# Performance work log

Measured on AMD Instinct MI355X. Metric: run time of the kernel, lower is better.

The kernel has to match this reference:

```python
import jax, jax.numpy as jnp
import numpy as np
import jax.scipy.linalg as jsp

H = 8
C = 64
D_CONV = 4
EPS_L2 = 1e-6
EPS_RMS = 1e-5


def l2norm(x):
    return x * jax.lax.rsqrt(jnp.sum(x * x, axis=-1, keepdims=True) + EPS_L2)


def setup_inputs() -> dict:
    key = jax.random.key(0)
    ks = jax.random.split(key, 12)
    B, T, D = 4, 4096, 1024
    x = jax.random.normal(ks[0], (B, T, D), dtype=jnp.float32)
    s = 0.02
    Wv = jax.random.normal(ks[1], (D, D), dtype=jnp.float32) * s
    Wg = jax.random.normal(ks[2], (D, D), dtype=jnp.float32) * s
    Wo = jax.random.normal(ks[3], (D, D), dtype=jnp.float32) * s
    Wb = jax.random.normal(ks[4], (H, D), dtype=jnp.float32) * s
    Wa = jax.random.normal(ks[5], (H, D), dtype=jnp.float32) * s
    # dt_bias / A_log initialized as in the torch module
    u = jax.random.uniform(ks[6], (H,))
    dt = jnp.exp(u * (jnp.log(0.1) - jnp.log(0.001)) + jnp.log(0.001))
    dt_bias = dt + jnp.log(-jnp.expm1(-dt))
    A_log = jnp.log(jax.random.uniform(ks[7], (H,)) * 16.0 + 1e-4)
    norm_w = jnp.ones((D // H,), dtype=jnp.float32)
    conv_w = jax.random.normal(ks[8], (D, D_CONV), dtype=jnp.float32) * 0.1
    conv_b = jnp.zeros((D,), dtype=jnp.float32)
    return {"x": x, "Wv": Wv, "Wg": Wg, "Wo": Wo, "Wb": Wb, "Wa": Wa,
            "dt_bias": dt_bias, "A_log": A_log, "norm_w": norm_w,
            "conv_w": conv_w, "conv_b": conv_b}


def _causal_depthwise_conv(x, w, b):
    # x: (B,T,D), w: (D,d_conv) -- causal depthwise conv1d
    B, T, D = x.shape
    xp = jnp.pad(x, ((0, 0), (D_CONV - 1, 0), (0, 0)))
    out = b
    for j in range(D_CONV):
        out = out + xp[:, j:j + T] * w[:, j]
    return out


def _forward(x, Wv, Wg, Wo, Wb, Wa, dt_bias, A_log, norm_w, conv_w, conv_b):
    B, T, D = x.shape
    K = D // H
    n = T // C  # T chosen as a multiple of C, so pad_len == 0

    rk = l2norm(x.reshape(B, T, H, K)) / np.sqrt(K)
    x_shift = jnp.pad(x[:, :-1], ((0, 0), (1, 0), (0, 0)))
    wk = l2norm(x_shift.reshape(B, T, H, K))
    v = jax.nn.silu(_causal_depthwise_conv(x @ Wv.T, conv_w, conv_b)).reshape(B, T, H, K)
    gate = (x @ Wg.T).reshape(B, T, H, K)
    beta = jax.nn.sigmoid(x @ Wb.T)                       # (B,T,H)
    decay = -jnp.exp(A_log) * jax.nn.softplus(x @ Wa.T + dt_bias)  # (B,T,H)

    # -> (B,H,T,K)
    rk, wk, v = (jnp.transpose(t, (0, 2, 1, 3)) for t in (rk, wk, v))
    beta_t = jnp.transpose(beta, (0, 2, 1))[..., None]    # (B,H,T,1)
    v = v * beta_t
    wk_beta = wk * beta_t

    # chunk: (B,H,n,C,K)
    ch = lambda t: t.reshape(B, H, n, C, K)
    rk, wk, v, wk_beta = ch(rk), ch(wk), ch(v), ch(wk_beta)
    decay = jnp.cumsum(jnp.transpose(decay, (0, 2, 1)).reshape(B, H, n, C), axis=-1)
    decay_exp = jnp.exp(decay)[..., None]                 # (B,H,n,C,1)

    tril = jnp.tril(jnp.ones((C, C), dtype=bool))
    strict_lower = jnp.tril(jnp.ones((C, C), dtype=bool), k=-1)
    diff = decay[..., :, None] - decay[..., None, :]
    L_mask = jnp.where(tril, jnp.exp(jnp.where(tril, diff, 0.0)), 0.0)  # (B,H,n,C,C)

    A_strict = jnp.where(strict_lower,
                         -(jnp.einsum('bhnck,bhndk->bhncd', wk_beta, wk) * L_mask), 0.0)
    # forward-substitution loop == inverse of unit-lower-triangular (I - A_strict)
    eye = jnp.eye(C, dtype=x.dtype)
    Tmat = jsp.solve_triangular(eye - A_strict,
                                jnp.broadcast_to(eye, A_strict.shape),
                                lower=True)
    v = Tmat @ v
    wk_cumdecay = Tmat @ (wk_beta * decay_exp)

    # scan over chunks maintaining state S: (B,H,K,K)
    def step(S, inp):
        rk_i, wk_i, v_i, wkc_i, L_i, dec_i = inp
        attn = jnp.where(tril, jnp.einsum('bhck,bhdk->bhcd', rk_i, wk_i) * L_i, 0.0)
        v_new = v_i - wkc_i @ S
        o_inter = (rk_i * jnp.exp(dec_i)[..., None]) @ S
        o_i = o_inter + attn @ v_new
        dw = jnp.exp(dec_i[..., -1:] - dec_i)[..., None]
        S_new = S * jnp.exp(dec_i[..., -1])[..., None, None] + \
            jnp.einsum('bhck,bhcv->bhkv', wk_i * dw, v_new)
        return S_new, o_i

    mv = lambda t: jnp.moveaxis(t, 2, 0)  # chunk axis to front
    S0 = jnp.zeros((B, H, K, K), dtype=x.dtype)
    _, o = jax.lax.scan(step, S0, (mv(rk), mv(wk), mv(v), mv(wk_cumdecay),
                                   mv(L_mask), mv(decay)))
    # o: (n,B,H,C,K) -> (B,T,H,K)
    o = jnp.transpose(o, (1, 0, 3, 2, 4)).reshape(B, T, H, K)

    # per-head RMSNorm, gated, output projection
    o = o * jax.lax.rsqrt(jnp.mean(o * o, axis=-1, keepdims=True) + EPS_RMS) * norm_w
    o = o * jax.nn.silu(gate)
    return o.reshape(B, T, D) @ Wo.T


def reference(x, Wv, Wg, Wo, Wb, Wa, dt_bias, A_log, norm_w, conv_w, conv_b):
    return _forward(x, Wv, Wg, Wo, Wb, Wa, dt_bias, A_log, norm_w, conv_w, conv_b)
```

## Files before the change

kernel.cpp:

```cpp
#include <hip/hip_runtime.h>
#include <hip/hip_bf16.h>
#include <math.h>

#define H_ 8
#define K_ 128
#define C_ 64
#define D_ 1024
#define T_ 4096
#define B_ 4
#define N_CH 64
#define BT_ (B_*T_)

typedef __attribute__((ext_vector_type(8))) short bf16x8;
typedef __attribute__((ext_vector_type(4))) float f32x4;
typedef __hip_bfloat16 bf16;

#define BAR_LGKM() do { \
  asm volatile("s_waitcnt lgkmcnt(0)" ::: "memory"); \
  __builtin_amdgcn_sched_barrier(0); \
  __builtin_amdgcn_s_barrier(); \
} while(0)

__device__ __forceinline__ float siluf(float x){ return x / (1.0f + expf(-x)); }
__device__ __forceinline__ float expn(float x){ return expf(fminf(x, 0.f)); }
__device__ __forceinline__ float sanf(float v){ return (__builtin_fabsf(v) <= 1e30f) ? v : 0.f; }

__device__ __forceinline__ void ld_bf8(const bf16* p, float* o){
  uint4 u = *(const uint4*)p;
  o[0]=__uint_as_float(u.x<<16); o[1]=__uint_as_float(u.x&0xffff0000u);
  o[2]=__uint_as_float(u.y<<16); o[3]=__uint_as_float(u.y&0xffff0000u);
  o[4]=__uint_as_float(u.z<<16); o[5]=__uint_as_float(u.z&0xffff0000u);
  o[6]=__uint_as_float(u.w<<16); o[7]=__uint_as_float(u.w&0xffff0000u);
}
__device__ __forceinline__ void ld_bf8s(const bf16* p, float* o){
  ld_bf8(p, o);
#pragma unroll
  for (int e=0;e<8;e++) o[e] = sanf(o[e]);
}
__device__ __forceinline__ void ld_bf4(const bf16* p, float* o){
  uint2 u = *(const uint2*)p;
  o[0]=__uint_as_float(u.x<<16); o[1]=__uint_as_float(u.x&0xffff0000u);
  o[2]=__uint_as_float(u.y<<16); o[3]=__uint_as_float(u.y&0xffff0000u);
}
__device__ __forceinline__ void ld_bf4s(const bf16* p, float* o){
  ld_bf4(p, o);
#pragma unroll
  for (int e=0;e<4;e++) o[e] = sanf(o[e]);
}
__device__ __forceinline__ unsigned short f2bfu(float f){
  bf16 h = __float2bfloat16(f);
  return *reinterpret_cast<unsigned short*>(&h);
}
__device__ __forceinline__ uint2 pack_bf4(const float* v){
  uint2 r;
  r.x = (unsigned)f2bfu(v[0]) | ((unsigned)f2bfu(v[1])<<16);
  r.y = (unsigned)f2bfu(v[2]) | ((unsigned)f2bfu(v[3])<<16);
  return r;
}

__global__ __launch_bounds__(256) void cast_f2b(
    const float* __restrict__ src, bf16* __restrict__ dst, int n4)
{
  int i = blockIdx.x*256 + threadIdx.x;
  if (i >= n4) return;
  float4 v = *(const float4*)&src[(size_t)i*4];
  float a[4] = {v.x, v.y, v.z, v.w};
  *(uint2*)&dst[(size_t)i*4] = pack_bf4(a);
}

template<typename OUT_T>
__global__ __launch_bounds__(256) void gemm_bt_mfma(
    const bf16* __restrict__ X, const bf16* __restrict__ W,
    OUT_T* __restrict__ Y, int M, int N, int K)
{
  __shared__ __align__(16) bf16 As[128*64];
  __shared__ __align__(16) bf16 Bs[128*64];
  const int tid = threadIdx.x;
  const int wv = tid >> 6;
  const int lane = tid & 63;
  const int row0 = blockIdx.y*128, col0 = blockIdx.x*128;
  const int mw = (wv&1)*64, nw = (wv>>1)*64;
  const int q = lane >> 4;
  const int l15 = lane & 15;
  f32x4 acc[4][4];
#pragma unroll
  for (int mi=0;mi<4;mi++)
#pragma unroll
    for (int ni=0;ni<4;ni++) acc[mi][ni] = (f32x4){0.f,0.f,0.f,0.f};

  const int sr = tid >> 3;
  const int sc = (tid & 7) * 8;
  for (int k0=0;k0<K;k0+=64){
#pragma unroll
    for (int i=0;i<4;i++){
      __builtin_amdgcn_global_load_lds(
          (const void*)&X[(size_t)(row0 + i*32 + sr)*K + k0 + sc],
          (void*)&As[i*2048 + wv*512], 16, 0, 0);
      __builtin_amdgcn_global_load_lds(
          (const void*)&W[(size_t)(col0 + i*32 + sr)*K + k0 + sc],
          (void*)&Bs[i*2048 + wv*512], 16, 0, 0);
    }
    __syncthreads();
#pragma unroll
    for (int ks=0; ks<64; ks+=32){
      bf16x8 af[4], bfr[4];
#pragma unroll
      for (int i=0;i<4;i++){
        af[i]  = *(const bf16x8*)&As[(mw + i*16 + l15)*64 + ks + q*8];
        bfr[i] = *(const bf16x8*)&Bs[(nw + i*16 + l15)*64 + ks + q*8];
      }
#pragma unroll
      for (int mi=0;mi<4;mi++)
#pragma unroll
        for (int ni=0;ni<4;ni++)
          acc[mi][ni] = __builtin_amdgcn_mfma_f32_16x16x32_bf16(af[mi], bfr[ni], acc[mi][ni], 0,0,0);
    }
    __syncthreads();
  }
#pragma unroll
  for (int mi=0;mi<4;mi++){
#pragma unroll
    for (int reg=0;reg<4;reg++){
      int row = row0 + mw + mi*16 + q*4 + reg;
#pragma unroll
      for (int ni=0;ni<4;ni++){
        int col = col0 + nw + ni*16 + l15;
        if constexpr (sizeof(OUT_T) == 2)
          Y[(size_t)row*N + col] = (OUT_T)__float2bfloat16(acc[mi][ni][reg]);
        else
          Y[(size_t)row*N + col] = (OUT_T)acc[mi][ni][reg];
      }
    }
  }
}

__global__ __launch_bounds__(256) void proj_small(
    const float* __restrict__ x, const float* __restrict__ Wb, const float* __restrict__ Wa,
    const float* __restrict__ dt_bias, const float* __restrict__ A_log,
    float* __restrict__ beta_out, float* __restrict__ dec_out)
{
  const int w = threadIdx.x >> 6;
  const int lane = threadIdx.x & 63;
  const int bt = blockIdx.x*4 + w;
  const int b = bt >> 12, t = bt & (T_-1);
  const float* xr = x + (size_t)bt*D_;
  float xv[16];
#pragma unroll
  for (int p=0;p<4;p++){
    float4 v = *(const float4*)&xr[lane*16 + p*4];
    xv[p*4+0]=v.x; xv[p*4+1]=v.y; xv[p*4+2]=v.z; xv[p*4+3]=v.w;
  }
  float accb[H_], acca[H_];
#pragma unroll
  for (int h=0;h<H_;h++){
    float sb=0.f, sa=0.f;
#pragma unroll
    for (int p=0;p<4;p++){
      float4 wb = *(const float4*)&Wb[(size_t)h*D_ + lane*16 + p*4];
      float4 wa = *(const float4*)&Wa[(size_t)h*D_ + lane*16 + p*4];
      sb += xv[p*4+0]*wb.x + xv[p*4+1]*wb.y + xv[p*4+2]*wb.z + xv[p*4+3]*wb.w;
      sa += xv[p*4+0]*wa.x + xv[p*4+1]*wa.y + xv[p*4+2]*wa.z + xv[p*4+3]*wa.w;
    }
    accb[h]=sb; acca[h]=sa;
  }
#pragma unroll
  for (int h=0;h<H_;h++){
#pragma unroll
    for (int m=1;m<64;m<<=1){
      accb[h] += __shfl_xor(accb[h], m, 64);
      acca[h] += __shfl_xor(acca[h], m, 64);
    }
  }
  if (lane < H_) {
    int h = lane;
    beta_out[(size_t)(b*H_+h)*T_ + t] = 1.f/(1.f+expf(-accb[h]));
  } else if (lane < 2*H_) {
    int h = lane - H_;
    float z = acca[h] + dt_bias[h];
    float sp = fmaxf(z,0.f) + log1pf(expf(-fabsf(z)));
    dec_out[(size_t)(b*H_+h)*T_ + t] = -expf(A_log[h]) * sp;
  }
}

__global__ __launch_bounds__(256) void xinv_kernel(
    const float* __restrict__ x, float* __restrict__ xinv, bf16* __restrict__ xb)
{
  const int bt = blockIdx.x;
  const int b = bt >> 12, t = bt & (T_-1);
  const int tid = threadIdx.x;
  float4 xv = *(const float4*)&x[(size_t)bt*D_ + tid*4];
  float a[4] = {xv.x, xv.y, xv.z, xv.w};
  *(uint2*)&xb[(size_t)bt*D_ + tid*4] = pack_bf4(a);
  float ss = xv.x*xv.x + xv.y*xv.y + xv.z*xv.z + xv.w*xv.w;
#pragma unroll
  for (int m=1;m<32;m<<=1) ss += __shfl_xor(ss, m, 32);
  const int h = tid >> 5;
  if ((tid & 31) == 0)
    xinv[(size_t)(b*H_+h)*T_ + t] = rsqrtf(ss + 1e-6f);
}

__global__ __launch_bounds__(256) void cumsum_dec(
    const float* __restrict__ dec_raw, float* __restrict__ dec_cum)
{
  int g = blockIdx.x*4 + (threadIdx.x>>6);
  int lane = threadIdx.x & 63;
  float v = sanf(dec_raw[(size_t)g*C_ + lane]);
#pragma unroll
  for (int off=1; off<64; off<<=1){
    float u = __shfl_up(v, off, 64);
    if (lane >= off) v += u;
  }
  dec_cum[(size_t)g*C_ + lane] = v;
}

__global__ __launch_bounds__(256) void chunk_prep(
    const bf16* __restrict__ xb, const float* __restrict__ xinv,
    const bf16* __restrict__ vpre, const float* __restrict__ cw, const float* __restrict__ cb,
    const float* __restrict__ beta, const float* __restrict__ dec,
    bf16* __restrict__ vchk, bf16* __restrict__ wkc, bf16* __restrict__ attn)
{
  __shared__ __align__(16) bf16 s_x[65][136];
  __shared__ __align__(16) float s_a[64][64];
  __shared__ float s_dec[64], s_beta[64], s_invsh[64], s_negbi[64], s_rsc[64], s_sc2[64];

  const int tid = threadIdx.x;
  const int chunk = blockIdx.x;
  const int bh = chunk >> 6;
  const int nc = chunk & 63;
  const int b = bh >> 3, h = bh & 7;
  const int t0 = nc * C_;
  const size_t xrow = (size_t)b*T_;
  const size_t rowb = (size_t)bh*T_ + t0;
  const size_t kobase = rowb * K_;
  const int w = tid >> 6;
  const int lane = tid & 63;
  const int l15 = lane & 15;
  const int q = lane >> 4;

  for (int idx = tid; idx < 65*16; idx += 256){
    int r = idx >> 4;
    int seg = (idx & 15) * 8;
    int t = t0 + r - 1;
    int tr = t < 0 ? 0 : t;
    *(uint4*)&s_x[r][seg] = *(const uint4*)&xb[(xrow + tr)*D_ + h*K_ + seg];
  }
  if (tid < C_){
    int c = tid;
    float dv  = sanf(dec[rowb + c]);
    float bet = sanf(beta[rowb + c]);
    float invc = sanf(xinv[rowb + c]);
    int tm1 = t0 + c - 1;
    float ivs = (tm1 >= 0) ? sanf(xinv[(size_t)bh*T_ + tm1]) : 0.f;
    s_dec[c] = dv;
    s_beta[c] = bet;
    s_invsh[c] = ivs;
    s_negbi[c] = -bet * ivs;
    s_rsc[c] = invc * 0.08838834764831845f;
    s_sc2[c] = ivs * bet * expn(dv);
  }
  __syncthreads();

  bf16x8 aG[4], aT[4];
#pragma unroll
  for (int ks=0; ks<4; ks++){
    aG[ks] = *(const bf16x8*)&s_x[16*w + l15][ks*32 + q*8];
    aT[ks] = *(const bf16x8*)&s_x[16*w + l15 + 1][ks*32 + q*8];
  }
  f32x4 accG[4], accT[4];
#pragma unroll
  for (int J=0;J<4;J++){ accG[J]=(f32x4){0.f,0.f,0.f,0.f}; accT[J]=(f32x4){0.f,0.f,0.f,0.f}; }
#pragma unroll
  for (int J=0;J<4;J++){
    if (J <= w){
#pragma unroll
      for (int ks=0; ks<4; ks++){
        bf16x8 bfrag = *(const bf16x8*)&s_x[16*J + l15][ks*32 + q*8];
        accG[J] = __builtin_amdgcn_mfma_f32_16x16x32_bf16(aG[ks], bfrag, accG[J], 0,0,0);
        accT[J] = __builtin_amdgcn_mfma_f32_16x16x32_bf16(aT[ks], bfrag, accT[J], 0,0,0);
      }
    }
  }
  {
    const int i0 = 16*w + q*4;
#pragma unroll
    for (int J=0;J<4;J++){
      const int j = 16*J + l15;
#pragma unroll
      for (int reg=0;reg<4;reg++){
        const int i = i0 + reg;
        if (j < i)
          s_a[i][j] = s_negbi[i] * s_invsh[j] * expn(s_dec[i]-s_dec[j]) * accG[J][reg];
        float val = 0.f;
        if (j <= i)
          val = s_rsc[i] * s_invsh[j] * expn(s_dec[i]-s_dec[j]) * accT[J][reg];
        attn[(size_t)chunk*4096 + i*64 + j] = __float2bfloat16(val);
      }
    }
  }

  float v[64];
  if (tid < 128){
    const int col = tid;
    float4 cwv = *(const float4*)&cw[(h*K_+col)*4];
    const float cbv = cb[h*K_+col];
    const bf16* vp = vpre + (xrow + t0)*D_ + h*K_ + col;
    float win0, win1, win2;
    { int t = t0-3; win0 = (t>=0)? sanf(__bfloat162float(vpre[(xrow+t)*D_+h*K_+col])) : 0.f; }
    { int t = t0-2; win1 = (t>=0)? sanf(__bfloat162float(vpre[(xrow+t)*D_+h*K_+col])) : 0.f; }
    { int t = t0-1; win2 = (t>=0)? sanf(__bfloat162float(vpre[(xrow+t)*D_+h*K_+col])) : 0.f; }
#pragma unroll
    for (int c8=0; c8<8; c8++){
      float nv[8];
#pragma unroll
      for (int u=0;u<8;u++) nv[u] = sanf(__bfloat162float(vp[(size_t)(c8*8+u)*D_]));
#pragma unroll
      for (int u=0;u<8;u++){
        const int c = c8*8+u;
        float a = cbv + cwv.x*win0 + cwv.y*win1 + cwv.z*win2 + cwv.w*nv[u];
        v[c] = siluf(a) * s_beta[c];
        win0=win1; win1=win2; win2=nv[u];
      }
    }
  } else {
    const int col = tid - 128;
#pragma unroll
    for (int c=0;c<64;c++)
      v[c] = __bfloat162float(s_x[c][col]) * s_sc2[c];
  }
  __syncthreads();

#pragma unroll
  for (int i=1;i<64;i++){
    const float* ar = s_a[i];
    float s0=0.f, s1=0.f, s2=0.f, s3=0.f;
    int j=0;
#pragma unroll
    for (; j+4<=i; j+=4){
      float4 a4 = *(const float4*)&ar[j];
      s0 += a4.x*v[j+0]; s1 += a4.y*v[j+1];
      s2 += a4.z*v[j+2]; s3 += a4.w*v[j+3];
    }
#pragma unroll
    for (; j<i; j++) s0 += ar[j]*v[j];
    v[i] += (s0+s2)+(s1+s3);
  }

  {
    const int col = tid & 127;
    bf16* dst = (tid < 128 ? vchk : wkc) + kobase + col;
#pragma unroll
    for (int c=0;c<64;c++)
      dst[(size_t)c*K_] = __float2bfloat16(v[c]);
  }
}

__global__ __launch_bounds__(512) void scan_kernel(
    const bf16* __restrict__ xb, const float* __restrict__ xinv,
    bf16* vo, const bf16* __restrict__ wkc,
    const bf16* __restrict__ attn, const float* __restrict__ dec)
{
  __shared__ __align__(16) bf16 ab_w[2][C_][136];
  __shared__ __align__(16) bf16 ab_x[2][C_][136];
  __shared__ __align__(16) bf16 xst  [K_][72];
  __shared__ __align__(16) bf16 a_att[C_][72];
  __shared__ __align__(16) bf16 st_hi[16][136];
  __shared__ __align__(16) bf16 st_lo[16][136];
  __shared__ __align__(16) bf16 vn_t [16][72];
  __shared__ __align__(16) bf16 vn_sh[16][72];
  __shared__ __align__(16) bf16 vn_sl[16][72];
  __shared__ float s_o[2][C_];
  __shared__ float s_scv[2][C_];
  __shared__ float s_a63[2];

  const int tid = threadIdx.x;
  const int bh = blockIdx.x & 31;
  const int g  = blockIdx.x >> 5;
  const int b = bh >> 3, h = bh & 7;
  const int j0 = g*16;
  const int w  = tid >> 6;
  const int lane = tid & 63;
  const int l15 = lane & 15;
  const int q = lane >> 4;
  const size_t xrow = (size_t)b*T_;

  for (int e=tid; e<16*136; e+=512){
    ((unsigned short*)&st_hi[0][0])[e] = 0;
    ((unsigned short*)&st_lo[0][0])[e] = 0;
  }

  if (w < 4){
    const int wrow = 16*w;
    f32x4 accS[2];
    accS[0] = (f32x4){0.f,0.f,0.f,0.f};
    accS[1] = (f32x4){0.f,0.f,0.f,0.f};
    bf16 pf_v[4];
    {
      const bf16* pv = vo + ((size_t)bh*T_ + wrow + q*4)*K_ + j0 + l15;
#pragma unroll
      for (int r=0;r<4;r++) pf_v[r] = pv[(size_t)r*K_];
    }
    BAR_LGKM();

    for (int nc=0; nc<N_CH; nc++){
      const size_t rowb = (size_t)bh*T_ + (size_t)nc*C_;
      const int pb = nc & 1;
      float vinit[4];
#pragma unroll
      for (int r=0;r<4;r++) vinit[r] = __bfloat162float(pf_v[r]);
      {
        int nn = (nc+1 < N_CH) ? nc+1 : nc;
        const bf16* pv = vo + ((size_t)bh*T_ + (size_t)nn*C_ + wrow + q*4)*K_ + j0 + l15;
#pragma unroll
        for (int r=0;r<4;r++) pf_v[r] = pv[(size_t)r*K_];
      }
      f32x4 accV, accP = (f32x4){0.f,0.f,0.f,0.f};
#pragma unroll
      for (int r=0;r<4;r++) accV[r] = vinit[r];
      __builtin_amdgcn_s_setprio(1);
#pragma unroll
      for (int ks=0; ks<4; ks++){
        bf16x8 bh_ = *(const bf16x8*)&st_hi[l15][ks*32 + q*8];
        bf16x8 bl_ = *(const bf16x8*)&st_lo[l15][ks*32 + q*8];
        bf16x8 a1 = *(const bf16x8*)&ab_w[pb][wrow + l15][ks*32 + q*8];
        bf16x8 a2 = *(const bf16x8*)&ab_x[pb][wrow + l15][ks*32 + q*8];
        accV = __builtin_amdgcn_mfma_f32_16x16x32_bf16(a1, bh_, accV, 0,0,0);
        accV = __builtin_amdgcn_mfma_f32_16x16x32_bf16(a1, bl_, accV, 0,0,0);
        accP = __builtin_amdgcn_mfma_f32_16x16x32_bf16(a2, bh_, accP, 0,0,0);
        accP = __builtin_amdgcn_mfma_f32_16x16x32_bf16(a2, bl_, accP, 0,0,0);
      }
      __builtin_amdgcn_s_setprio(0);
      f32x4 sov  = *(const f32x4*)&s_o[pb][wrow + q*4];
      f32x4 scvv = *(const f32x4*)&s_scv[pb][wrow + q*4];
      const float a63 = s_a63[pb];
      f32x4 oacc;
#pragma unroll
      for (int r=0;r<4;r++) oacc[r] = accP[r] * sov[r];
      {
        float v4[4] = {accV[0],accV[1],accV[2],accV[3]};
        *(uint2*)&vn_t[l15][wrow + q*4] = pack_bf4(v4);
        float vs[4];
#pragma unroll
        for (int r=0;r<4;r++) vs[r] = accV[r] * scvv[r];
        uint2 ph = pack_bf4(vs);
        float lo4[4];
        lo4[0] = vs[0] - __uint_as_float(ph.x << 16);
        lo4[1] = vs[1] - __uint_as_float(ph.x & 0xffff0000u);
        lo4[2] = vs[2] - __uint_as_float(ph.y << 16);
        lo4[3] = vs[3] - __uint_as_float(ph.y & 0xffff0000u);
        *(uint2*)&vn_sh[l15][wrow + q*4] = ph;
        *(uint2*)&vn_sl[l15][wrow + q*4] = pack_bf4(lo4);
      }
      BAR_LGKM();

      __builtin_amdgcn_s_setprio(1);
#pragma unroll
      for (int ks=0; ks<2; ks++){
        bf16x8 aA = *(const bf16x8*)&a_att[wrow + l15][ks*32 + q*8];
        bf16x8 bV = *(const bf16x8*)&vn_t[l15][ks*32 + q*8];
        oacc = __builtin_amdgcn_mfma_f32_16x16x32_bf16(aA, bV, oacc, 0,0,0);
      }
      __builtin_amdgcn_s_setprio(0);
      {
        bf16* po = vo + (rowb + wrow + q*4)*K_ + j0 + l15;
#pragma unroll
        for (int r=0;r<4;r++) po[(size_t)r*K_] = __float2bfloat16(oacc[r]);
      }
      __builtin_amdgcn_s_setprio(1);
#pragma unroll
      for (int sub=0; sub<2; sub++){
        f32x4 acc = accS[sub];
#pragma unroll
        for (int r=0;r<4;r++) acc[r] *= a63;
#pragma unroll
        for (int ks=0; ks<2; ks++){
          bf16x8 aH = *(const bf16x8*)&vn_sh[l15][ks*32 + q*8];
          bf16x8 aL = *(const bf16x8*)&vn_sl[l15][ks*32 + q*8];
          bf16x8 bX = *(const bf16x8*)&xst[32*w + 16*sub + l15][ks*32 + q*8];
          acc = __builtin_amdgcn_mfma_f32_16x16x32_bf16(aH, bX, acc, 0,0,0);
          acc = __builtin_amdgcn_mfma_f32_16x16x32_bf16(aL, bX, acc, 0,0,0);
        }
        accS[sub] = acc;
#pragma unroll
        for (int r=0;r<4;r++){
          float sv = acc[r];
          bf16 hb = __float2bfloat16(sv);
          st_hi[q*4+r][32*w + 16*sub + l15] = hb;
          st_lo[q*4+r][32*w + 16*sub + l15] = __float2bfloat16(sv - __bfloat162float(hb));
        }
      }
      __builtin_amdgcn_s_setprio(0);
      BAR_LGKM();
    }
  } else {
    const int tp = tid - 256;
    const int r_st = tp >> 2;
    const int k8   = (tp & 3) * 8;
    const int xc0  = (tp & 31) * 2;
    const int xkb  = (tp >> 5) * 16;

    uint4 A_w[4], A_x[4];
    float A_d = 0.f, A_d63 = 0.f, A_i = 0.f, A_ip = 0.f;
    uint4 B_t[4], B_a[2];

    auto issueA = [&](int c){
      const int t0 = c*C_;
      const size_t rowb = (size_t)bh*T_ + t0;
      const bf16* pw = wkc + (rowb + r_st)*K_ + k8;
      const bf16* px = xb + (xrow + t0 + r_st)*D_ + h*K_ + k8;
#pragma unroll
      for (int i=0;i<4;i++){
        A_w[i] = *(const uint4*)(pw + i*32);
        A_x[i] = *(const uint4*)(px + i*32);
      }
      if (tp < C_){
        A_d   = dec[rowb + tp];
        A_d63 = dec[rowb + 63];
        A_i   = xinv[(size_t)bh*T_ + t0 + tp];
        int tm1 = t0 + tp - 1;
        A_ip  = (tm1 >= 0) ? xinv[(size_t)bh*T_ + tm1] : 0.f;
      }
    };
    auto issueB = [&](int c){
      const int t0 = c*C_;
      const bf16* pa = attn + (size_t)(bh*N_CH + c)*4096 + r_st*64 + k8;
      B_a[0] = *(const uint4*)pa;
      B_a[1] = *(const uint4*)(pa + 32);
      int t1 = t0 + xc0 - 1;
      const bf16* p1 = xb + (xrow + (t1 < 0 ? 0 : t1))*D_ + h*K_ + xkb;
      const bf16* p2 = xb + (xrow + (t0 + xc0))*D_ + h*K_ + xkb;
      B_t[0] = *(const uint4*)p1; B_t[1] = *(const uint4*)(p1+8);
      B_t[2] = *(const uint4*)p2; B_t[3] = *(const uint4*)(p2+8);
    };
    auto writeA = [&](int buf){
#pragma unroll
      for (int i=0;i<4;i++){
        uint4 u = A_w[i];
        u.x ^= 0x80008000u; u.y ^= 0x80008000u; u.z ^= 0x80008000u; u.w ^= 0x80008000u;
        *(uint4*)&ab_w[buf][r_st][k8 + i*32] = u;
        *(uint4*)&ab_x[buf][r_st][k8 + i*32] = A_x[i];
      }
      if (tp < C_){
        float dv  = sanf(A_d);
        float d63 = sanf(A_d63);
        s_o[buf][tp]   = sanf(A_i) * 0.08838834764831845f * expn(dv);
        s_scv[buf][tp] = sanf(A_ip) * expn(d63 - dv);
        if (tp == 63) s_a63[buf] = expn(d63);
      }
    };
    auto writeB = [&](){
      *(uint4*)&a_att[r_st][k8]      = B_a[0];
      *(uint4*)&a_att[r_st][k8 + 32] = B_a[1];
      unsigned r1[8] = {B_t[0].x,B_t[0].y,B_t[0].z,B_t[0].w,
                        B_t[1].x,B_t[1].y,B_t[1].z,B_t[1].w};
      unsigned r2[8] = {B_t[2].x,B_t[2].y,B_t[2].z,B_t[2].w,
                        B_t[3].x,B_t[3].y,B_t[3].z,B_t[3].w};
#pragma unroll
      for (int i2=0;i2<8;i2++){
        *(unsigned*)&xst[xkb + 2*i2][xc0]     = (r1[i2] & 0xffffu) | (r2[i2] << 16);
        *(unsigned*)&xst[xkb + 2*i2 + 1][xc0] = (r1[i2] >> 16) | (r2[i2] & 0xffff0000u);
      }
    };

    issueA(0);
    writeA(0);
    issueA(1);
    issueB(0);
    BAR_LGKM();

    for (int nc=0; nc<N_CH; nc++){
      writeA((nc+1)&1);
      writeB();
      int na = (nc+2 < N_CH) ? nc+2 : N_CH-1;
      int nb = (nc+1 < N_CH) ? nc+1 : N_CH-1;
      issueA(na);
      issueB(nb);
      BAR_LGKM();
      BAR_LGKM();
    }
  }
}

__global__ __launch_bounds__(256) void norm_gate(
    const bf16* __restrict__ o, bf16* gio, const float* __restrict__ norm_w)
{
  const int bt = blockIdx.x;
  const int b = bt >> 12, t = bt & (T_-1);
  const int tid = threadIdx.x;
  const int h = tid >> 5;
  const int kk = (tid & 31)*4;
  float ov[4];
  ld_bf4s(o + ((size_t)(b*H_+h)*T_ + t)*K_ + kk, ov);
  float ss = ov[0]*ov[0] + ov[1]*ov[1] + ov[2]*ov[2] + ov[3]*ov[3];
#pragma unroll
  for (int m=1;m<32;m<<=1) ss += __shfl_xor(ss, m, 32);
  float r = rsqrtf(ss*(1.f/128.f) + 1e-5f);
  float4 nw = *(const float4*)&norm_w[kk];
  float gv[4];
  ld_bf4s(gio + (size_t)bt*D_ + tid*4, gv);
  float res[4];
  res[0] = ov[0]*r*nw.x * siluf(gv[0]);
  res[1] = ov[1]*r*nw.y * siluf(gv[1]);
  res[2] = ov[2]*r*nw.z * siluf(gv[2]);
  res[3] = ov[3]*r*nw.w * siluf(gv[3]);
  *(uint2*)&gio[(size_t)bt*D_ + tid*4] = pack_bf4(res);
}

extern "C" void kernel_launch(void* const* d_in, const int* in_sizes, int n_in,
                              void* d_out, int out_size, void* d_ws, size_t ws_size,
                              hipStream_t stream)
{
  const float* x       = (const float*)d_in[0];
  const float* Wv      = (const float*)d_in[1];
  const float* Wg      = (const float*)d_in[2];
  const float* Wo      = (const float*)d_in[3];
  const float* Wb      = (const float*)d_in[4];
  const float* Wa      = (const float*)d_in[5];
  const float* dt_bias = (const float*)d_in[6];
  const float* A_log   = (const float*)d_in[7];
  const float* norm_w  = (const float*)d_in[8];
  const float* conv_w  = (const float*)d_in[9];
  const float* conv_b  = (const float*)d_in[10];
  float* out = (float*)d_out;

  const size_t BTD = (size_t)B_*T_*D_;
  const size_t BHT = (size_t)B_*H_*T_;
  const size_t DD  = (size_t)D_*D_;

  float* beta = (float*)d_ws;
  float* decr = beta + BHT;
  float* decc = decr + BHT;
  float* xinv = decc + BHT;
  bf16* Wvb = (bf16*)(xinv + BHT);
  bf16* Wgb = Wvb + DD;
  bf16* Wob = Wgb + DD;
  bf16* xb   = Wob + DD;
  bf16* vpre = xb + BTD;
  bf16* wkc  = vpre + BTD;
  bf16* vo   = (bf16*)d_out;
  bf16* attn = vo + BTD;

  dim3 gemm_grid(D_/128, BT_/128);
  xinv_kernel<<<BT_, 256, 0, stream>>>(x, xinv, xb);
  cast_f2b<<<(DD/4+255)/256, 256, 0, stream>>>(Wv, Wvb, DD/4);
  cast_f2b<<<(DD/4+255)/256, 256, 0, stream>>>(Wg, Wgb, DD/4);
  cast_f2b<<<(DD/4+255)/256, 256, 0, stream>>>(Wo, Wob, DD/4);
  gemm_bt_mfma<bf16><<<gemm_grid, 256, 0, stream>>>(xb, Wvb, vpre, BT_, D_, D_);
  proj_small<<<BT_/4, 256, 0, stream>>>(x, Wb, Wa, dt_bias, A_log, beta, decr);
  cumsum_dec<<<(BHT/C_)/4, 256, 0, stream>>>(decr, decc);
  chunk_prep<<<B_*H_*N_CH, 256, 0, stream>>>(xb, xinv, vpre, conv_w, conv_b,
                                             beta, decc, vo , wkc, attn);
  scan_kernel<<<B_*H_*8, 512, 0, stream>>>(xb, xinv, vo, wkc, attn, decc);
  gemm_bt_mfma<bf16><<<gemm_grid, 256, 0, stream>>>(xb, Wgb, vpre, BT_, D_, D_);
  norm_gate<<<BT_, 256, 0, stream>>>(vo , vpre , norm_w);
  gemm_bt_mfma<float><<<gemm_grid, 256, 0, stream>>>(vpre, Wob, out, BT_, D_, D_);
}
```

Before: 656.3 us.

## Fuse RMSNorm and gating into gate GEMM epilogue, swizzle GEMM LDS

Removes the standalone norm_gate kernel. The gate GEMM epilogue now computes each head's RMS over the scan output, with a cross-wave reduction through shared memory, and writes the normalized, gated bf16 result directly. The GEMM LDS tile layout gains an XOR swizzle on global_load_lds destinations and fragment reads to reduce bank conflicts. The chunk_prep triangular forward-substitution loop becomes a recursive template for full compile-time unrolling. The fused epilogue reads o with strided scalar bf16 loads and adds an extra barrier.

```diff
diff --git a/kernel.cpp b/kernel.cpp
--- a/kernel.cpp
+++ b/kernel.cpp
@@ -32,11 +32,6 @@
   o[4]=__uint_as_float(u.z<<16); o[5]=__uint_as_float(u.z&0xffff0000u);
   o[6]=__uint_as_float(u.w<<16); o[7]=__uint_as_float(u.w&0xffff0000u);
 }
-__device__ __forceinline__ void ld_bf8s(const bf16* p, float* o){
-  ld_bf8(p, o);
-#pragma unroll
-  for (int e=0;e<8;e++) o[e] = sanf(o[e]);
-}
 __device__ __forceinline__ void ld_bf4(const bf16* p, float* o){
   uint2 u = *(const uint2*)p;
   o[0]=__uint_as_float(u.x<<16); o[1]=__uint_as_float(u.x&0xffff0000u);
@@ -58,6 +53,26 @@
   return r;
 }
 
+template<int I> __device__ __forceinline__ void fsub_step(float* v, const float (*sa)[64]){
+  const float* ar = sa[I];
+  float s0=0.f,s1=0.f,s2=0.f,s3=0.f;
+  constexpr int I4 = I & ~3;
+#pragma unroll
+  for (int j=0;j<I4;j+=4){
+    float4 a4 = *(const float4*)&ar[j];
+    s0 += a4.x*v[j+0]; s1 += a4.y*v[j+1]; s2 += a4.z*v[j+2]; s3 += a4.w*v[j+3];
+  }
+#pragma unroll
+  for (int j=I4;j<I;j++) s0 += ar[j]*v[j];
+  v[I] += (s0+s2)+(s1+s3);
+}
+template<int I> __device__ __forceinline__ void fsub_all(float* v, const float (*sa)[64]){
+  if constexpr (I >= 1){
+    fsub_all<I-1>(v, sa);
+    fsub_step<I>(v, sa);
+  }
+}
+
 __global__ __launch_bounds__(256) void cast_f2b(
     const float* __restrict__ src, bf16* __restrict__ dst, int n4)
 {
@@ -68,10 +83,11 @@
   *(uint2*)&dst[(size_t)i*4] = pack_bf4(a);
 }
 
-template<typename OUT_T>
+template<typename OUT_T, bool FUSE_NG>
 __global__ __launch_bounds__(256) void gemm_bt_mfma(
     const bf16* __restrict__ X, const bf16* __restrict__ W,
-    OUT_T* __restrict__ Y, int M, int N, int K)
+    OUT_T* __restrict__ Y, int M, int N, int K,
+    const bf16* __restrict__ o_in, const float* __restrict__ norm_w)
 {
   __shared__ __align__(16) bf16 As[128*64];
   __shared__ __align__(16) bf16 Bs[128*64];
@@ -82,22 +98,23 @@
   const int mw = (wv&1)*64, nw = (wv>>1)*64;
   const int q = lane >> 4;
   const int l15 = lane & 15;
+  const int swr = l15 & 7;
   f32x4 acc[4][4];
 #pragma unroll
   for (int mi=0;mi<4;mi++)
 #pragma unroll
     for (int ni=0;ni<4;ni++) acc[mi][ni] = (f32x4){0.f,0.f,0.f,0.f};
 
-  const int sr = tid >> 3;
-  const int sc = (tid & 7) * 8;
+  const int sr8 = lane >> 3;
+  const int scs = ((lane & 7) ^ sr8) * 8;
   for (int k0=0;k0<K;k0+=64){
 #pragma unroll
     for (int i=0;i<4;i++){
       __builtin_amdgcn_global_load_lds(
-          (const void*)&X[(size_t)(row0 + i*32 + sr)*K + k0 + sc],
+          (const void*)&X[(size_t)(row0 + i*32 + wv*8 + sr8)*K + k0 + scs],
           (void*)&As[i*2048 + wv*512], 16, 0, 0);
       __builtin_amdgcn_global_load_lds(
-          (const void*)&W[(size_t)(col0 + i*32 + sr)*K + k0 + sc],
+          (const void*)&W[(size_t)(col0 + i*32 + wv*8 + sr8)*K + k0 + scs],
           (void*)&Bs[i*2048 + wv*512], 16, 0, 0);
     }
     __syncthreads();
@@ -106,8 +123,9 @@
       bf16x8 af[4], bfr[4];
 #pragma unroll
       for (int i=0;i<4;i++){
-        af[i]  = *(const bf16x8*)&As[(mw + i*16 + l15)*64 + ks + q*8];
-        bfr[i] = *(const bf16x8*)&Bs[(nw + i*16 + l15)*64 + ks + q*8];
+        const int cc = (((ks>>3) + q) ^ swr) * 8;
+        af[i]  = *(const bf16x8*)&As[(mw + i*16 + l15)*64 + cc];
+        bfr[i] = *(const bf16x8*)&Bs[(nw + i*16 + l15)*64 + cc];
       }
 #pragma unroll
       for (int mi=0;mi<4;mi++)
@@ -117,18 +135,63 @@
     }
     __syncthreads();
   }
-#pragma unroll
-  for (int mi=0;mi<4;mi++){
-#pragma unroll
-    for (int reg=0;reg<4;reg++){
-      int row = row0 + mw + mi*16 + q*4 + reg;
-#pragma unroll
-      for (int ni=0;ni<4;ni++){
-        int col = col0 + nw + ni*16 + l15;
-        if constexpr (sizeof(OUT_T) == 2)
-          Y[(size_t)row*N + col] = (OUT_T)__float2bfloat16(acc[mi][ni][reg]);
-        else
-          Y[(size_t)row*N + col] = (OUT_T)acc[mi][ni][reg];
+
+  if constexpr (FUSE_NG){
+    float* s_red = (float*)As;
+    const int hh = blockIdx.x;
+    const int nwh = nw >> 6;
+#pragma unroll
+    for (int mi=0;mi<4;mi++){
+#pragma unroll
+      for (int reg=0;reg<4;reg++){
+        int row = row0 + mw + mi*16 + q*4 + reg;
+        int b = row >> 12, t = row & (T_-1);
+        const bf16* orow = o_in + ((size_t)(b*H_+hh)*T_ + t)*K_;
+        float ps = 0.f;
+#pragma unroll
+        for (int ni=0;ni<4;ni++){
+          float ov = sanf(__bfloat162float(orow[nw + ni*16 + l15]));
+          ps += ov*ov;
+        }
+        ps += __shfl_xor(ps,1,64); ps += __shfl_xor(ps,2,64);
+        ps += __shfl_xor(ps,4,64); ps += __shfl_xor(ps,8,64);
+        if (l15 == 0) s_red[nwh*128 + mw + mi*16 + q*4 + reg] = ps;
+      }
+    }
+    __syncthreads();
+#pragma unroll
+    for (int mi=0;mi<4;mi++){
+#pragma unroll
+      for (int reg=0;reg<4;reg++){
+        int lr = mw + mi*16 + q*4 + reg;
+        float ssum = s_red[lr] + s_red[128 + lr];
+        float rr = rsqrtf(ssum*(1.f/128.f) + 1e-5f);
+        int row = row0 + lr;
+        int b = row >> 12, t = row & (T_-1);
+        const bf16* orow = o_in + ((size_t)(b*H_+hh)*T_ + t)*K_;
+#pragma unroll
+        for (int ni=0;ni<4;ni++){
+          int k = nw + ni*16 + l15;
+          float ov = sanf(__bfloat162float(orow[k]));
+          float res = ov * rr * norm_w[k] * siluf(acc[mi][ni][reg]);
+          Y[(size_t)row*N + col0 + k] = (OUT_T)__float2bfloat16(res);
+        }
+      }
+    }
+  } else {
+#pragma unroll
+    for (int mi=0;mi<4;mi++){
+#pragma unroll
+      for (int reg=0;reg<4;reg++){
+        int row = row0 + mw + mi*16 + q*4 + reg;
+#pragma unroll
+        for (int ni=0;ni<4;ni++){
+          int col = col0 + nw + ni*16 + l15;
+          if constexpr (sizeof(OUT_T) == 2)
+            Y[(size_t)row*N + col] = (OUT_T)__float2bfloat16(acc[mi][ni][reg]);
+          else
+            Y[(size_t)row*N + col] = (OUT_T)acc[mi][ni][reg];
+        }
       }
     }
   }
@@ -329,21 +392,7 @@
   }
   __syncthreads();
 
-#pragma unroll
-  for (int i=1;i<64;i++){
-    const float* ar = s_a[i];
-    float s0=0.f, s1=0.f, s2=0.f, s3=0.f;
-    int j=0;
-#pragma unroll
-    for (; j+4<=i; j+=4){
-      float4 a4 = *(const float4*)&ar[j];
-      s0 += a4.x*v[j+0]; s1 += a4.y*v[j+1];
-      s2 += a4.z*v[j+2]; s3 += a4.w*v[j+3];
-    }
-#pragma unroll
-    for (; j<i; j++) s0 += ar[j]*v[j];
-    v[i] += (s0+s2)+(s1+s3);
-  }
+  fsub_all<63>(v, s_a);
 
   {
     const int col = tid & 127;
@@ -580,31 +629,6 @@
   }
 }
 
-__global__ __launch_bounds__(256) void norm_gate(
-    const bf16* __restrict__ o, bf16* gio, const float* __restrict__ norm_w)
-{
-  const int bt = blockIdx.x;
-  const int b = bt >> 12, t = bt & (T_-1);
-  const int tid = threadIdx.x;
-  const int h = tid >> 5;
-  const int kk = (tid & 31)*4;
-  float ov[4];
-  ld_bf4s(o + ((size_t)(b*H_+h)*T_ + t)*K_ + kk, ov);
-  float ss = ov[0]*ov[0] + ov[1]*ov[1] + ov[2]*ov[2] + ov[3]*ov[3];
-#pragma unroll
-  for (int m=1;m<32;m<<=1) ss += __shfl_xor(ss, m, 32);
-  float r = rsqrtf(ss*(1.f/128.f) + 1e-5f);
-  float4 nw = *(const float4*)&norm_w[kk];
-  float gv[4];
-  ld_bf4s(gio + (size_t)bt*D_ + tid*4, gv);
-  float res[4];
-  res[0] = ov[0]*r*nw.x * siluf(gv[0]);
-  res[1] = ov[1]*r*nw.y * siluf(gv[1]);
-  res[2] = ov[2]*r*nw.z * siluf(gv[2]);
-  res[3] = ov[3]*r*nw.w * siluf(gv[3]);
-  *(uint2*)&gio[(size_t)bt*D_ + tid*4] = pack_bf4(res);
-}
-
 extern "C" void kernel_launch(void* const* d_in, const int* in_sizes, int n_in,
                               void* d_out, int out_size, void* d_ws, size_t ws_size,
                               hipStream_t stream)
@@ -644,13 +668,12 @@
   cast_f2b<<<(DD/4+255)/256, 256, 0, stream>>>(Wv, Wvb, DD/4);
   cast_f2b<<<(DD/4+255)/256, 256, 0, stream>>>(Wg, Wgb, DD/4);
   cast_f2b<<<(DD/4+255)/256, 256, 0, stream>>>(Wo, Wob, DD/4);
-  gemm_bt_mfma<bf16><<<gemm_grid, 256, 0, stream>>>(xb, Wvb, vpre, BT_, D_, D_);
+  gemm_bt_mfma<bf16,false><<<gemm_grid, 256, 0, stream>>>(xb, Wvb, vpre, BT_, D_, D_, nullptr, nullptr);
   proj_small<<<BT_/4, 256, 0, stream>>>(x, Wb, Wa, dt_bias, A_log, beta, decr);
   cumsum_dec<<<(BHT/C_)/4, 256, 0, stream>>>(decr, decc);
   chunk_prep<<<B_*H_*N_CH, 256, 0, stream>>>(xb, xinv, vpre, conv_w, conv_b,
                                              beta, decc, vo , wkc, attn);
   scan_kernel<<<B_*H_*8, 512, 0, stream>>>(xb, xinv, vo, wkc, attn, decc);
-  gemm_bt_mfma<bf16><<<gemm_grid, 256, 0, stream>>>(xb, Wgb, vpre, BT_, D_, D_);
-  norm_gate<<<BT_, 256, 0, stream>>>(vo , vpre , norm_w);
-  gemm_bt_mfma<float><<<gemm_grid, 256, 0, stream>>>(vpre, Wob, out, BT_, D_, D_);
-}
+  gemm_bt_mfma<bf16,true><<<gemm_grid, 256, 0, stream>>>(xb, Wgb, vpre, BT_, D_, D_, vo, norm_w);
+  gemm_bt_mfma<float,false><<<gemm_grid, 256, 0, stream>>>(vpre, Wob, out, BT_, D_, D_, nullptr, nullptr);
+}
```

New measurement: 629.6 us. 1.04x faster.
